# Optimization experiments

Hardware: AMD Instinct MI355X
Metric: run time of the kernel (lower is better)

Reference implementation:

```python
import jax, jax.numpy as jnp
import numpy as np

B, S, D, H = 4, 2048, 1024, 16
HD = D // H  # head dim = 64


def setup_inputs() -> dict:
    key = jax.random.key(0)
    ks = jax.random.split(key, 9)
    scale = 1.0 / np.sqrt(D)
    inputs = jax.random.normal(ks[0], (B, S, D), dtype=jnp.float32)
    # causal lower-triangular mask, dim==2 -> broadcast [1,1,S,S] in self-attention branch
    mask = jnp.tril(jnp.ones((S, S), dtype=bool))
    Wq = jax.random.normal(ks[1], (D, D), dtype=jnp.float32) * scale
    bq = jnp.zeros((D,), dtype=jnp.float32)
    Wk = jax.random.normal(ks[2], (D, D), dtype=jnp.float32) * scale
    bk = jnp.zeros((D,), dtype=jnp.float32)
    Wv = jax.random.normal(ks[3], (D, D), dtype=jnp.float32) * scale
    bv = jnp.zeros((D,), dtype=jnp.float32)
    Wo = jax.random.normal(ks[4], (D, D), dtype=jnp.float32) * scale
    bo = jnp.zeros((D,), dtype=jnp.float32)
    return {"inputs": inputs, "mask": mask, "Wq": Wq, "bq": bq, "Wk": Wk,
            "bk": bk, "Wv": Wv, "bv": bv, "Wo": Wo, "bo": bo}


def reference(inputs, mask, Wq, bq, Wk, bk, Wv, bv, Wo, bo):
    # Dropout is identity in eval mode (reference baseline).
    b, s, _ = inputs.shape
    q = (inputs @ Wq.T + bq).reshape(b, s, H, HD).transpose(0, 2, 1, 3)  # [b,h,s,hd]
    k = (inputs @ Wk.T + bk).reshape(b, s, H, HD).transpose(0, 2, 1, 3)
    v = (inputs @ Wv.T + bv).reshape(b, s, H, HD).transpose(0, 2, 1, 3)
    scores = jnp.einsum('bhqd,bhkd->bhqk', q, k) / jnp.sqrt(jnp.float32(HD))
    scores = jnp.where(mask[None, None, :, :], scores, jnp.float32(-1e9))
    attn = jax.nn.softmax(scores, axis=-1)
    z = jnp.einsum('bhqk,bhkd->bhqd', attn, v)          # [b,h,s,hd]
    z = z.transpose(0, 2, 1, 3).reshape(b, s, H * HD)   # [b,s,D]
    return z @ Wo.T + bo
```

## Files before the change

### kernel.cpp

```cpp
#include <hip/hip_runtime.h>

#define Bn 4
#define Sn 2048
#define Dn 1024
#define Hn 16
#define HDn 64
#define MROWS (Bn * Sn)

typedef __attribute__((ext_vector_type(4))) float f32x4;
typedef __attribute__((ext_vector_type(8))) _Float16 f16x8;
typedef __attribute__((ext_vector_type(4))) _Float16 f16x4;
typedef unsigned int u32;

__device__ inline void gld_lds16(const void* g, void* l) {
    __builtin_amdgcn_global_load_lds(
        (const __attribute__((address_space(1))) u32*)g,
        (__attribute__((address_space(3))) u32*)l, 16, 0, 0);
}

__global__ __launch_bounds__(256)
void w2h(const float* __restrict__ q, const float* __restrict__ k,
         const float* __restrict__ v, const float* __restrict__ o,
         _Float16* __restrict__ out)
{
    const int i = blockIdx.x * 256 + threadIdx.x;
    const float* src = (blockIdx.y == 0) ? q : (blockIdx.y == 1) ? k
                     : (blockIdx.y == 2) ? v : o;
    const float4 x = ((const float4*)src)[i];
    f16x4 h;
    h[0] = (_Float16)x.x; h[1] = (_Float16)x.y;
    h[2] = (_Float16)x.z; h[3] = (_Float16)x.w;
    ((f16x4*)(out + (size_t)blockIdx.y * Dn * Dn))[i] = h;
}

__global__ __launch_bounds__(256)
void x2h(const float* __restrict__ in, _Float16* __restrict__ out)
{
    const int i = blockIdx.x * 256 + threadIdx.x;
    const float4 x = ((const float4*)in)[i];
    f16x4 h;
    h[0] = (_Float16)x.x; h[1] = (_Float16)x.y;
    h[2] = (_Float16)x.z; h[3] = (_Float16)x.w;
    ((f16x4*)out)[i] = h;
}

__global__ __launch_bounds__(256)
void gemm_qkv(const _Float16* __restrict__ Ah16, const _Float16* __restrict__ Wh,
              const float* __restrict__ bq, const float* __restrict__ bk,
              const float* __restrict__ bv, _Float16* __restrict__ Qh,
              _Float16* __restrict__ Kh, _Float16* __restrict__ Vt)
{
    __shared__ __align__(16) _Float16 As[128 * 32];
    __shared__ __align__(16) _Float16 Bs[128 * 32];
    const int tid = threadIdx.x;
    const int lane = tid & 63;
    const int w = tid >> 6;
    const int l15 = lane & 15, lg = lane >> 4;
    const int wr = w >> 1, wc = w & 1;

    const int d  = (int)blockIdx.x;
    const int wu = (d & 7) * 192 + (d >> 3);
    const int m0 = (wu / 24) * 128;
    const int n0 = (wu % 24) * 128;

    f32x4 acc[4][4];
#pragma unroll
    for (int mi = 0; mi < 4; ++mi)
#pragma unroll
        for (int ni = 0; ni < 4; ++ni) acc[mi][ni] = (f32x4){0.f, 0.f, 0.f, 0.f};

    const int rsub = lane >> 2;
    const int sch  = (lane & 3) ^ ((lane >> 2) & 3) ^ ((lane >> 4) & 3);
    const int fsw  = (l15 & 3) ^ ((l15 >> 2) & 3);

    for (int k0 = 0; k0 < Dn; k0 += 32) {
        __syncthreads();
#pragma unroll
        for (int i = 0; i < 2; ++i) {
            const int row = w * 32 + i * 16 + rsub;
            gld_lds16(Ah16 + (size_t)(m0 + row) * Dn + k0 + sch * 8,
                      &As[(w * 32 + i * 16) * 32]);
            gld_lds16(Wh + (size_t)(n0 + row) * Dn + k0 + sch * 8,
                      &Bs[(w * 32 + i * 16) * 32]);
        }
        __syncthreads();

        f16x8 af[4];
#pragma unroll
        for (int mi = 0; mi < 4; ++mi) {
            const int ar = wr * 64 + mi * 16 + l15;
            af[mi] = *(const f16x8*)&As[ar * 32 + ((lg ^ fsw) << 3)];
        }
#pragma unroll
        for (int ni = 0; ni < 4; ++ni) {
            const int br = wc * 64 + ni * 16 + l15;
            const f16x8 bf = *(const f16x8*)&Bs[br * 32 + ((lg ^ fsw) << 3)];
#pragma unroll
            for (int mi = 0; mi < 4; ++mi)
                acc[mi][ni] = __builtin_amdgcn_mfma_f32_16x16x32_f16(af[mi], bf, acc[mi][ni], 0, 0, 0);
        }
    }

    const int mat = n0 >> 10;
    const float* bias = (mat == 0) ? bq : (mat == 1) ? bk : bv;
#pragma unroll
    for (int ni = 0; ni < 4; ++ni) {
        const int col = n0 + wc * 64 + ni * 16 + l15;
        const int cmod = col & 1023;
        const float bcol = bias[cmod];
        const int hh = cmod >> 6, dd = cmod & 63;
#pragma unroll
        for (int mi = 0; mi < 4; ++mi) {
            const int mb = m0 + wr * 64 + mi * 16 + (lg << 2);
            const int ss = mb & (Sn - 1);
            const int bb = mb >> 11;
            if (mat == 0) {
#pragma unroll
                for (int r = 0; r < 4; ++r) {
                    const size_t ad = ((((size_t)bb * Hn + hh) * Sn + (ss + r)) << 6) + dd;
                    Qh[ad] = (_Float16)((acc[mi][ni][r] + bcol) * 0.125f);
                }
            } else if (mat == 1) {
#pragma unroll
                for (int r = 0; r < 4; ++r) {
                    const size_t ad = ((((size_t)bb * Hn + hh) * Sn + (ss + r)) << 6) + dd;
                    Kh[ad] = (_Float16)(acc[mi][ni][r] + bcol);
                }
            } else {
                f16x4 hv;
                hv[0] = (_Float16)(acc[mi][ni][0] + bcol);
                hv[1] = (_Float16)(acc[mi][ni][1] + bcol);
                hv[2] = (_Float16)(acc[mi][ni][2] + bcol);
                hv[3] = (_Float16)(acc[mi][ni][3] + bcol);
                const size_t ad = (((size_t)bb * Hn + hh) * HDn + dd) * Sn + ss;
                *(f16x4*)&Vt[ad] = hv;
            }
        }
    }
}

__global__ __launch_bounds__(256)
void gemm_out(const float* __restrict__ A, const _Float16* __restrict__ Wh,
              const float* __restrict__ bias, float* __restrict__ Cf)
{
    __shared__ __align__(16) _Float16 Ah[128 * 32];
    __shared__ __align__(16) _Float16 Al[128 * 32];
    __shared__ __align__(16) _Float16 Bs[128 * 32];
    const int tid = threadIdx.x;
    const int lane = tid & 63;
    const int w = tid >> 6;
    const int l15 = lane & 15, lg = lane >> 4;
    const int wr = w >> 1, wc = w & 1;
    const int n0 = blockIdx.x * 128, m0 = blockIdx.y * 128;

    f32x4 acc[4][4];
#pragma unroll
    for (int mi = 0; mi < 4; ++mi)
#pragma unroll
        for (int ni = 0; ni < 4; ++ni) acc[mi][ni] = (f32x4){0.f, 0.f, 0.f, 0.f};

    const int brsub = lane >> 2;
    const int bch = (lane & 3) ^ ((lane >> 2) & 3) ^ ((lane >> 4) & 3);
    const int fsw = (l15 & 3) ^ ((l15 >> 2) & 3);

    for (int k0 = 0; k0 < Dn; k0 += 32) {
        __syncthreads();
#pragma unroll
        for (int c = 0; c < 2; ++c) {
            const int rb = (w * 2 + c) * 16;
            const size_t gsrc = (size_t)(n0 + rb + brsub) * Dn + k0 + bch * 8;
            gld_lds16(Wh + gsrc, &Bs[rb * 32]);
        }
#pragma unroll
        for (int it = 0; it < 4; ++it) {
            const int qi = tid + (it << 8);
            const int row = qi >> 3, qc = qi & 7;
            const float4 v = *(const float4*)&A[(size_t)(m0 + row) * Dn + k0 + qc * 4];
            f16x4 h4, l4;
            h4[0] = (_Float16)v.x; l4[0] = (_Float16)(v.x - (float)h4[0]);
            h4[1] = (_Float16)v.y; l4[1] = (_Float16)(v.y - (float)h4[1]);
            h4[2] = (_Float16)v.z; l4[2] = (_Float16)(v.z - (float)h4[2]);
            h4[3] = (_Float16)v.w; l4[3] = (_Float16)(v.w - (float)h4[3]);
            const int sw = (qc >> 1) ^ (row & 3) ^ ((row >> 2) & 3);
            const int off = row * 32 + sw * 8 + (qc & 1) * 4;
            *(f16x4*)&Ah[off] = h4;
            *(f16x4*)&Al[off] = l4;
        }
        __syncthreads();

        f16x8 ah[4], al[4];
#pragma unroll
        for (int mi = 0; mi < 4; ++mi) {
            const int ar = wr * 64 + mi * 16 + l15;
            const int off = ar * 32 + ((lg ^ fsw) << 3);
            ah[mi] = *(const f16x8*)&Ah[off];
            al[mi] = *(const f16x8*)&Al[off];
        }
#pragma unroll
        for (int ni = 0; ni < 4; ++ni) {
            const int br = wc * 64 + ni * 16 + l15;
            const f16x8 bh = *(const f16x8*)&Bs[br * 32 + ((lg ^ fsw) << 3)];
#pragma unroll
            for (int mi = 0; mi < 4; ++mi) {
                acc[mi][ni] = __builtin_amdgcn_mfma_f32_16x16x32_f16(ah[mi], bh, acc[mi][ni], 0, 0, 0);
                acc[mi][ni] = __builtin_amdgcn_mfma_f32_16x16x32_f16(al[mi], bh, acc[mi][ni], 0, 0, 0);
            }
        }
    }

#pragma unroll
    for (int ni = 0; ni < 4; ++ni) {
        const int col = n0 + wc * 64 + ni * 16 + l15;
        const float bcol = bias[col];
#pragma unroll
        for (int mi = 0; mi < 4; ++mi) {
            const int mb = m0 + wr * 64 + mi * 16 + (lg << 2);
#pragma unroll
            for (int r = 0; r < 4; ++r)
                Cf[(size_t)(mb + r) * Dn + col] = acc[mi][ni][r] + bcol;
        }
    }
}

__device__ inline void stage_half(const _Float16* __restrict__ gp, _Float16* lb,
                                  bool isK, int t0, int half, int rsub, int sch)
{
#pragma unroll
    for (int i = 0; i < 4; ++i) {
        const int row = half * 32 + i * 8 + rsub;
        const _Float16* s_ = isK
            ? (gp + (size_t)(t0 + row) * HDn + sch * 8)
            : (gp + (size_t)row * Sn + t0 + sch * 8);
        gld_lds16(s_, lb + (size_t)(half * 32 + i * 8) * 64);
    }
}

__global__ __launch_bounds__(256, 3)
void attn_fwd(const _Float16* __restrict__ Qh, const _Float16* __restrict__ Kh,
              const _Float16* __restrict__ Vt, float* __restrict__ Z)
{
    __shared__ __align__(16) _Float16 Ks[2][4096];
    __shared__ __align__(16) _Float16 Vs[2][4096];
    __shared__ __align__(16) _Float16 Ps[4][32 * 72];

    const int tid = threadIdx.x, lane = tid & 63, w = tid >> 6;
    const int l15 = lane & 15, lg = lane >> 4;

    const int d  = (int)blockIdx.x;
    const int wu = (d & 7) * 128 + (d >> 3);
    const int qb = 15 - (wu & 15);
    const int h  = (wu >> 4) & 15;
    const int b  = wu >> 8;
    const int q0b = qb << 7;

    const size_t khoff = ((size_t)(b * Hn + h) * Sn) * HDn;
    const size_t vhoff = ((size_t)(b * Hn + h) * HDn) * Sn;
    const _Float16* Qg = Qh + khoff;
    const _Float16* Kg = Kh + khoff;
    const _Float16* Vg = Vt + vhoff;

    const int rsub = lane >> 3;
    const int sch  = (lane & 7) ^ rsub;
    const bool isK = (w < 2);
    const int half = w & 1;
    const _Float16* gp = isK ? Kg : Vg;

    f16x8 qf[2][2];
#pragma unroll
    for (int miq = 0; miq < 2; ++miq) {
        const _Float16* qsrc = &Qg[(size_t)(q0b + w * 32 + miq * 16 + l15) * HDn + lg * 8];
        qf[miq][0] = *(const f16x8*)qsrc;
        qf[miq][1] = *(const f16x8*)(qsrc + 32);
    }

    f32x4 acc[2][4];
#pragma unroll
    for (int miq = 0; miq < 2; ++miq)
#pragma unroll
        for (int nt = 0; nt < 4; ++nt) acc[miq][nt] = (f32x4){0.f, 0.f, 0.f, 0.f};
    float psum[2][4];
#pragma unroll
    for (int miq = 0; miq < 2; ++miq)
#pragma unroll
        for (int r = 0; r < 4; ++r) psum[miq][r] = 0.f;

    _Float16* Pw = &Ps[w][0];
    const int xa = (lg ^ (l15 & 7)) << 3;
    const int xb = ((lg ^ (l15 & 7)) ^ 4) << 3;
    const int qlo_w = q0b + w * 32;
    const int ntiles = 2 * qb + 2;

    stage_half(gp, isK ? &Ks[0][0] : &Vs[0][0], isK, 0, half, rsub, sch);

    for (int t = 0; t < ntiles; ++t) {
        if (t + 1 < ntiles) {
            _Float16* sb = isK ? &Ks[(t & 1) ^ 1][0] : &Vs[(t & 1) ^ 1][0];
            stage_half(gp, sb, isK, (t + 1) << 6, half, rsub, sch);
            asm volatile("s_waitcnt vmcnt(4)" ::: "memory");
        } else {
            asm volatile("s_waitcnt vmcnt(0)" ::: "memory");
        }
        __builtin_amdgcn_s_barrier();
        __builtin_amdgcn_sched_barrier(0);

        const _Float16* Kc = &Ks[t & 1][0];
        const _Float16* Vc = &Vs[t & 1][0];
        const int t0k = t << 6;
        const bool act[2] = { t0k <= qlo_w + 15, t0k <= qlo_w + 31 };
        const bool need_mask = (t0k + 63 > qlo_w);

        f32x4 sv[2][4];
#pragma unroll
        for (int nt = 0; nt < 4; ++nt) {
            const int kr = (nt * 16 + l15) << 6;
            const f16x8 k0 = *(const f16x8*)&Kc[kr + xa];
            const f16x8 k1 = *(const f16x8*)&Kc[kr + xb];
            __builtin_amdgcn_s_setprio(1);
#pragma unroll
            for (int miq = 0; miq < 2; ++miq) {
                if (!act[miq]) continue;
                f32x4 s = (f32x4){0.f, 0.f, 0.f, 0.f};
                s = __builtin_amdgcn_mfma_f32_16x16x32_f16(qf[miq][0], k0, s, 0, 0, 0);
                s = __builtin_amdgcn_mfma_f32_16x16x32_f16(qf[miq][1], k1, s, 0, 0, 0);
                sv[miq][nt] = s;
            }
            __builtin_amdgcn_s_setprio(0);
        }

        if (need_mask) {
#pragma unroll
            for (int miq = 0; miq < 2; ++miq) {
                if (!act[miq]) continue;
#pragma unroll
                for (int nt = 0; nt < 4; ++nt) {
                    const int key = t0k + nt * 16 + l15;
#pragma unroll
                    for (int r = 0; r < 4; ++r) {
                        const int qq = qlo_w + miq * 16 + (lg << 2) + r;
                        if (key > qq) sv[miq][nt][r] = -1e30f;
                    }
                }
            }
        }

#pragma unroll
        for (int miq = 0; miq < 2; ++miq) {
            if (!act[miq]) continue;
#pragma unroll
            for (int nt = 0; nt < 4; ++nt) {
#pragma unroll
                for (int r = 0; r < 4; ++r) {
                    const float p = __expf(fminf(sv[miq][nt][r], 10.f));
                    sv[miq][nt][r] = p;
                    psum[miq][r] += p;
                }
#pragma unroll
                for (int r = 0; r < 4; ++r)
                    Pw[(miq * 16 + (lg << 2) + r) * 72 + nt * 16 + l15] =
                        (_Float16)sv[miq][nt][r];
            }
        }

        f16x8 pa[2][2];
#pragma unroll
        for (int miq = 0; miq < 2; ++miq)
            if (act[miq]) {
                pa[miq][0] = *(const f16x8*)&Pw[(miq * 16 + l15) * 72 + (lg << 3)];
                pa[miq][1] = *(const f16x8*)&Pw[(miq * 16 + l15) * 72 + 32 + (lg << 3)];
            }

#pragma unroll
        for (int nt = 0; nt < 4; ++nt) {
            const int vr = (nt * 16 + l15) << 6;
            const f16x8 v0 = *(const f16x8*)&Vc[vr + xa];
            const f16x8 v1 = *(const f16x8*)&Vc[vr + xb];
            __builtin_amdgcn_s_setprio(1);
#pragma unroll
            for (int miq = 0; miq < 2; ++miq) {
                if (!act[miq]) continue;
                acc[miq][nt] = __builtin_amdgcn_mfma_f32_16x16x32_f16(pa[miq][0], v0, acc[miq][nt], 0, 0, 0);
                acc[miq][nt] = __builtin_amdgcn_mfma_f32_16x16x32_f16(pa[miq][1], v1, acc[miq][nt], 0, 0, 0);
            }
            __builtin_amdgcn_s_setprio(0);
        }

        __builtin_amdgcn_sched_barrier(0);
        __builtin_amdgcn_s_barrier();
    }

#pragma unroll
    for (int miq = 0; miq < 2; ++miq)
#pragma unroll
        for (int r = 0; r < 4; ++r) {
            float rs = psum[miq][r];
            rs += __shfl_xor(rs, 1);
            rs += __shfl_xor(rs, 2);
            rs += __shfl_xor(rs, 4);
            rs += __shfl_xor(rs, 8);
            const float inv = 1.f / rs;
            const int qg = q0b + w * 32 + miq * 16 + (lg << 2) + r;
            float* dst = &Z[(size_t)(b * Sn + qg) * Dn + h * HDn];
#pragma unroll
            for (int nt = 0; nt < 4; ++nt)
                dst[nt * 16 + l15] = acc[miq][nt][r] * inv;
        }
}

extern "C" void kernel_launch(void* const* d_in, const int* in_sizes, int n_in,
                              void* d_out, int out_size, void* d_ws, size_t ws_size,
                              hipStream_t stream)
{
    const float* x  = (const float*)d_in[0];
    const float* Wq = (const float*)d_in[2];
    const float* bq = (const float*)d_in[3];
    const float* Wk = (const float*)d_in[4];
    const float* bk = (const float*)d_in[5];
    const float* Wv = (const float*)d_in[6];
    const float* bv = (const float*)d_in[7];
    const float* Wo = (const float*)d_in[8];
    const float* bo = (const float*)d_in[9];
    float* out = (float*)d_out;

    char* ws = (char*)d_ws;
    float*    Zf  = (float*)ws;
    _Float16* xh  = (_Float16*)(ws + 16777216);
    _Float16* Qh  = (_Float16*)(ws + 33554432);
    _Float16* Kh  = (_Float16*)(ws + 50331648);
    _Float16* VTh = (_Float16*)(ws + 67108864);
    _Float16* Whp = (_Float16*)(ws + 83886080);

    const int wn4 = Dn * Dn / 4;
    const size_t WN = (size_t)Dn * Dn;

    w2h<<<dim3(wn4 / 256, 4), 256, 0, stream>>>(Wq, Wk, Wv, Wo, Whp);
    x2h<<<dim3(MROWS * Dn / 4 / 256), 256, 0, stream>>>(x, xh);
    gemm_qkv<<<dim3(1536), 256, 0, stream>>>(xh, Whp, bq, bk, bv, Qh, Kh, VTh);

    attn_fwd<<<dim3(1024), 256, 0, stream>>>(Qh, Kh, VTh, Zf);

    gemm_out<<<dim3(Dn / 128, MROWS / 128), 256, 0, stream>>>(
        Zf, Whp + 3 * WN, bo, out);
}
```

Before: 234.0 us.

## Emit split fp16 hi/lo attention output and async-load it in out-projection

```diff
diff --git a/kernel.cpp b/kernel.cpp
--- a/kernel.cpp
+++ b/kernel.cpp
@@ -140,8 +140,9 @@
 }
 
 __global__ __launch_bounds__(256)
-void gemm_out(const float* __restrict__ A, const _Float16* __restrict__ Wh,
-              const float* __restrict__ bias, float* __restrict__ Cf)
+void gemm_out(const _Float16* __restrict__ Ahp, const _Float16* __restrict__ Alp,
+              const _Float16* __restrict__ Wh, const float* __restrict__ bias,
+              float* __restrict__ Cf)
 {
     __shared__ __align__(16) _Float16 Ah[128 * 32];
     __shared__ __align__(16) _Float16 Al[128 * 32];
@@ -151,7 +152,11 @@
     const int w = tid >> 6;
     const int l15 = lane & 15, lg = lane >> 4;
     const int wr = w >> 1, wc = w & 1;
-    const int n0 = blockIdx.x * 128, m0 = blockIdx.y * 128;
+
+    const int d  = (int)blockIdx.x;
+    const int wu = (d & 7) * 64 + (d >> 3);
+    const int m0 = (wu >> 3) * 128;
+    const int n0 = (wu & 7) * 128;
 
     f32x4 acc[4][4];
 #pragma unroll
@@ -159,32 +164,19 @@
 #pragma unroll
         for (int ni = 0; ni < 4; ++ni) acc[mi][ni] = (f32x4){0.f, 0.f, 0.f, 0.f};
 
-    const int brsub = lane >> 2;
-    const int bch = (lane & 3) ^ ((lane >> 2) & 3) ^ ((lane >> 4) & 3);
-    const int fsw = (l15 & 3) ^ ((l15 >> 2) & 3);
+    const int rsub = lane >> 2;
+    const int sch  = (lane & 3) ^ ((lane >> 2) & 3) ^ ((lane >> 4) & 3);
+    const int fsw  = (l15 & 3) ^ ((l15 >> 2) & 3);
 
     for (int k0 = 0; k0 < Dn; k0 += 32) {
         __syncthreads();
 #pragma unroll
-        for (int c = 0; c < 2; ++c) {
-            const int rb = (w * 2 + c) * 16;
-            const size_t gsrc = (size_t)(n0 + rb + brsub) * Dn + k0 + bch * 8;
-            gld_lds16(Wh + gsrc, &Bs[rb * 32]);
-        }
-#pragma unroll
-        for (int it = 0; it < 4; ++it) {
-            const int qi = tid + (it << 8);
-            const int row = qi >> 3, qc = qi & 7;
-            const float4 v = *(const float4*)&A[(size_t)(m0 + row) * Dn + k0 + qc * 4];
-            f16x4 h4, l4;
-            h4[0] = (_Float16)v.x; l4[0] = (_Float16)(v.x - (float)h4[0]);
-            h4[1] = (_Float16)v.y; l4[1] = (_Float16)(v.y - (float)h4[1]);
-            h4[2] = (_Float16)v.z; l4[2] = (_Float16)(v.z - (float)h4[2]);
-            h4[3] = (_Float16)v.w; l4[3] = (_Float16)(v.w - (float)h4[3]);
-            const int sw = (qc >> 1) ^ (row & 3) ^ ((row >> 2) & 3);
-            const int off = row * 32 + sw * 8 + (qc & 1) * 4;
-            *(f16x4*)&Ah[off] = h4;
-            *(f16x4*)&Al[off] = l4;
+        for (int i = 0; i < 2; ++i) {
+            const int row = w * 32 + i * 16 + rsub;
+            const int lb  = (w * 32 + i * 16) * 32;
+            gld_lds16(Ahp + (size_t)(m0 + row) * Dn + k0 + sch * 8, &Ah[lb]);
+            gld_lds16(Alp + (size_t)(m0 + row) * Dn + k0 + sch * 8, &Al[lb]);
+            gld_lds16(Wh  + (size_t)(n0 + row) * Dn + k0 + sch * 8, &Bs[lb]);
         }
         __syncthreads();
 
@@ -199,11 +191,11 @@
 #pragma unroll
         for (int ni = 0; ni < 4; ++ni) {
             const int br = wc * 64 + ni * 16 + l15;
-            const f16x8 bh = *(const f16x8*)&Bs[br * 32 + ((lg ^ fsw) << 3)];
+            const f16x8 bf = *(const f16x8*)&Bs[br * 32 + ((lg ^ fsw) << 3)];
 #pragma unroll
             for (int mi = 0; mi < 4; ++mi) {
-                acc[mi][ni] = __builtin_amdgcn_mfma_f32_16x16x32_f16(ah[mi], bh, acc[mi][ni], 0, 0, 0);
-                acc[mi][ni] = __builtin_amdgcn_mfma_f32_16x16x32_f16(al[mi], bh, acc[mi][ni], 0, 0, 0);
+                acc[mi][ni] = __builtin_amdgcn_mfma_f32_16x16x32_f16(ah[mi], bf, acc[mi][ni], 0, 0, 0);
+                acc[mi][ni] = __builtin_amdgcn_mfma_f32_16x16x32_f16(al[mi], bf, acc[mi][ni], 0, 0, 0);
             }
         }
     }
@@ -237,7 +229,8 @@
 
 __global__ __launch_bounds__(256, 3)
 void attn_fwd(const _Float16* __restrict__ Qh, const _Float16* __restrict__ Kh,
-              const _Float16* __restrict__ Vt, float* __restrict__ Z)
+              const _Float16* __restrict__ Vt, _Float16* __restrict__ Zh,
+              _Float16* __restrict__ Zl)
 {
     __shared__ __align__(16) _Float16 Ks[2][4096];
     __shared__ __align__(16) _Float16 Vs[2][4096];
@@ -399,10 +392,14 @@
             rs += __shfl_xor(rs, 8);
             const float inv = 1.f / rs;
             const int qg = q0b + w * 32 + miq * 16 + (lg << 2) + r;
-            float* dst = &Z[(size_t)(b * Sn + qg) * Dn + h * HDn];
-#pragma unroll
-            for (int nt = 0; nt < 4; ++nt)
-                dst[nt * 16 + l15] = acc[miq][nt][r] * inv;
+            const size_t base = (size_t)(b * Sn + qg) * Dn + h * HDn;
+#pragma unroll
+            for (int nt = 0; nt < 4; ++nt) {
+                const float o = acc[miq][nt][r] * inv;
+                const _Float16 oh = (_Float16)o;
+                Zh[base + nt * 16 + l15] = oh;
+                Zl[base + nt * 16 + l15] = (_Float16)(o - (float)oh);
+            }
         }
 }
 
@@ -422,7 +419,8 @@
     float* out = (float*)d_out;
 
     char* ws = (char*)d_ws;
-    float*    Zf  = (float*)ws;
+    _Float16* Zh  = (_Float16*)ws;
+    _Float16* Zl  = (_Float16*)(ws + 16777216);
     _Float16* xh  = (_Float16*)(ws + 16777216);
     _Float16* Qh  = (_Float16*)(ws + 33554432);
     _Float16* Kh  = (_Float16*)(ws + 50331648);
@@ -436,8 +434,7 @@
     x2h<<<dim3(MROWS * Dn / 4 / 256), 256, 0, stream>>>(x, xh);
     gemm_qkv<<<dim3(1536), 256, 0, stream>>>(xh, Whp, bq, bk, bv, Qh, Kh, VTh);
 
-    attn_fwd<<<dim3(1024), 256, 0, stream>>>(Qh, Kh, VTh, Zf);
-
-    gemm_out<<<dim3(Dn / 128, MROWS / 128), 256, 0, stream>>>(
-        Zf, Whp + 3 * WN, bo, out);
-}
+    attn_fwd<<<dim3(1024), 256, 0, stream>>>(Qh, Kh, VTh, Zh, Zl);
+
+    gemm_out<<<dim3(512), 256, 0, stream>>>(Zh, Zl, Whp + 3 * WN, bo, out);
+}
```

Measured after the change: 228.0 us. 1.03x faster.
